# Performance work log

Hardware: AMD Instinct MI355X
Metric: run time of the kernel (lower is better)

## Reference

```python
import jax, jax.numpy as jnp
import numpy as np

N, E, D = 100000, 600000, 128

def setup_inputs() -> dict:
    key = jax.random.key(0)
    ks = jax.random.split(key, 6)
    s = 1.0 / np.sqrt(D)
    return {
        "h": jax.random.normal(ks[0], (N, D), dtype=jnp.float32),
        "edge_index": jax.random.randint(ks[1], (2, E), 0, N, dtype=jnp.int64),
        "Wg": jax.random.normal(ks[2], (2 * D, D), dtype=jnp.float32) * s,
        "bg": jnp.zeros((D,), dtype=jnp.float32),
        "Ws": jax.random.normal(ks[3], (D, D), dtype=jnp.float32) * s,
        "bs": jnp.zeros((D,), dtype=jnp.float32),
        "Wr": jax.random.normal(ks[4], (D, D), dtype=jnp.float32) * s,
        "br": jnp.zeros((D,), dtype=jnp.float32),
    }

def reference(h, edge_index, Wg, bg, Ws, bs, Wr, br):
    send, rec = edge_index[0], edge_index[1]
    h_rec = h[rec]            # [E, D]
    h_send = h[send]          # [E, D]
    # gate: sigmoid(Linear(cat([h_rec, h_send])))  -- split W to avoid concat copy
    gate_in = h_rec @ Wg[:h.shape[1]] + h_send @ Wg[h.shape[1]:] + bg
    eta = jax.nn.sigmoid(gate_in)                      # [E, D]
    h_messages = eta * (h_send @ Ws + bs)              # [E, D]
    h_agg = jax.ops.segment_sum(h_messages, rec, num_segments=h.shape[0])
    return (h @ Wr + br) + h_agg
```

## Files before the change

### kernel.cpp

```cpp
#include <hip/hip_runtime.h>
#include <stdint.h>

#define FD 128

typedef __bf16 bf16x8 __attribute__((ext_vector_type(8)));
typedef unsigned short u16x8 __attribute__((ext_vector_type(8)));
typedef float  f32x16 __attribute__((ext_vector_type(16)));

__device__ __forceinline__ unsigned short f2bf(float f) {
    unsigned u = __float_as_uint(f);
    unsigned r = u + 0x7fffu + ((u >> 16) & 1u);
    return (unsigned short)(r >> 16);
}
__device__ __forceinline__ float bflo(unsigned u) { return __uint_as_float(u << 16); }
__device__ __forceinline__ float bfhi(unsigned u) { return __uint_as_float(u & 0xffff0000u); }

__global__ __launch_bounds__(256) void prep_kernel(
    const float* __restrict__ Wg,
    const float* __restrict__ Ws,
    const float* __restrict__ Wr,
    unsigned short* __restrict__ Wf)
{
    int wid = blockIdx.x * 256 + threadIdx.x;
    if (wid >= 512 * 128) return;
    int j  = wid & 7;
    int l  = (wid >> 3) & 63;
    int kt = (wid >> 9) & 7;
    int ct = wid >> 12;
    int k  = kt * 16 + (l >> 5) * 8 + j;
    int c  = ct * 32 + (l & 31);
    float v;
    if (c < 128)      v = Wg[k * FD + c];
    else if (c < 256) v = Wg[(128 + k) * FD + (c - 128)];
    else if (c < 384) v = Ws[k * FD + (c - 256)];
    else              v = Wr[k * FD + (c - 384)];
    Wf[wid] = f2bf(v);
}

__global__ __launch_bounds__(256, 2) void gemm_kernel(
    const float* __restrict__ h,
    const unsigned short* __restrict__ Wf,
    const float* __restrict__ bg,
    const float* __restrict__ bs,
    const float* __restrict__ br,
    unsigned short* __restrict__ A,
    unsigned short* __restrict__ B,
    unsigned short* __restrict__ S,
    float* __restrict__ out,
    int N)
{
    const int w    = threadIdx.x >> 6;
    const int lane = threadIdx.x & 63;
    const int rb   = blockIdx.x * 32;

    f32x16 acc[4];
    #pragma unroll
    for (int i = 0; i < 4; ++i)
        #pragma unroll
        for (int r = 0; r < 16; ++r) acc[i][r] = 0.0f;

    int arow = rb + (lane & 31);
    if (arow >= N) arow = N - 1;
    const float* aptr = h + (size_t)arow * FD + (lane >> 5) * 8;

    float4 raw[16];
    #pragma unroll
    for (int kt = 0; kt < 8; ++kt) {
        raw[2 * kt]     = *(const float4*)(aptr + kt * 16);
        raw[2 * kt + 1] = *(const float4*)(aptr + kt * 16 + 4);
    }

    bf16x8 afrag[8];
    #pragma unroll
    for (int kt = 0; kt < 8; ++kt) {
        union { u16x8 u; bf16x8 b; } cv;
        float4 f0 = raw[2 * kt];
        float4 f1 = raw[2 * kt + 1];
        cv.u[0] = f2bf(f0.x); cv.u[1] = f2bf(f0.y);
        cv.u[2] = f2bf(f0.z); cv.u[3] = f2bf(f0.w);
        cv.u[4] = f2bf(f1.x); cv.u[5] = f2bf(f1.y);
        cv.u[6] = f2bf(f1.z); cv.u[7] = f2bf(f1.w);
        afrag[kt] = cv.b;
    }

    const unsigned short* bbase = Wf + (size_t)(w * 4 * 8 * 64 + lane) * 8;
    #pragma unroll
    for (int kt = 0; kt < 8; ++kt) {
        #pragma unroll
        for (int i = 0; i < 4; ++i) {
            bf16x8 bfr = *(const bf16x8*)(bbase + (size_t)(i * 8 + kt) * 64 * 8);
            acc[i] = __builtin_amdgcn_mfma_f32_32x32x16_bf16(afrag[kt], bfr, acc[i], 0, 0, 0);
        }
    }

    const int col_l  = lane & 31;
    const int rhalf  = (lane >> 5) * 4;
    #pragma unroll
    for (int i = 0; i < 4; ++i) {
        int col = i * 32 + col_l;
        float bias = (w == 0) ? bg[col] : (w == 2) ? bs[col] : (w == 3) ? br[col] : 0.0f;
        #pragma unroll
        for (int r = 0; r < 16; ++r) {
            int row = rb + (r & 3) + 8 * (r >> 2) + rhalf;
            if (row < N) {
                float v = acc[i][r] + bias;
                size_t off = (size_t)row * FD + col;
                if (w == 0)      A[off] = f2bf(v);
                else if (w == 1) B[off] = f2bf(v);
                else if (w == 2) S[off] = f2bf(v);
                else             out[off] = v;
            }
        }
    }
}

__global__ __launch_bounds__(256) void hist_kernel(
    const int* __restrict__ idx, int* __restrict__ deg, int E)
{
    int e = blockIdx.x * 256 + threadIdx.x;
    if (e >= E) return;
    atomicAdd(&deg[idx[E + e]], 1);
}

__global__ __launch_bounds__(256) void scan1_kernel(
    const int* __restrict__ deg, int* __restrict__ partial, int N)
{
    __shared__ int sh[256];
    int base = blockIdx.x * 1024 + threadIdx.x * 4;
    int s = 0;
    #pragma unroll
    for (int j = 0; j < 4; ++j) s += (base + j < N) ? deg[base + j] : 0;
    sh[threadIdx.x] = s;
    __syncthreads();
    for (int ofs = 128; ofs > 0; ofs >>= 1) {
        if (threadIdx.x < ofs) sh[threadIdx.x] += sh[threadIdx.x + ofs];
        __syncthreads();
    }
    if (threadIdx.x == 0) partial[blockIdx.x] = sh[0];
}

__global__ __launch_bounds__(256) void scan2_kernel(int* __restrict__ partial, int nb)
{
    __shared__ int sh[256];
    int t = threadIdx.x;
    int p = (t < nb) ? partial[t] : 0;
    sh[t] = p;
    __syncthreads();
    for (int ofs = 1; ofs < 256; ofs <<= 1) {
        int x = (t >= ofs) ? sh[t - ofs] : 0;
        __syncthreads();
        sh[t] += x;
        __syncthreads();
    }
    if (t < nb) partial[t] = sh[t] - p;
}

__global__ __launch_bounds__(256) void scan3_kernel(
    int* __restrict__ deg, const int* __restrict__ partial, int N)
{
    __shared__ int sh[256];
    int base = blockIdx.x * 1024 + threadIdx.x * 4;
    int v[4];
    #pragma unroll
    for (int j = 0; j < 4; ++j) v[j] = (base + j < N) ? deg[base + j] : 0;
    int tsum = v[0] + v[1] + v[2] + v[3];
    sh[threadIdx.x] = tsum;
    __syncthreads();
    for (int ofs = 1; ofs < 256; ofs <<= 1) {
        int x = (threadIdx.x >= ofs) ? sh[threadIdx.x - ofs] : 0;
        __syncthreads();
        sh[threadIdx.x] += x;
        __syncthreads();
    }
    int run = partial[blockIdx.x] + sh[threadIdx.x] - tsum;
    #pragma unroll
    for (int j = 0; j < 4; ++j) {
        if (base + j < N) deg[base + j] = run;
        run += v[j];
    }
}

__global__ __launch_bounds__(256) void scatter_kernel(
    const int* __restrict__ idx, int* __restrict__ off,
    int* __restrict__ csr, int E)
{
    int e = blockIdx.x * 256 + threadIdx.x;
    if (e >= E) return;
    int s = idx[e];
    int r = idx[E + e];
    int pos = atomicAdd(&off[r], 1);
    csr[pos] = s;
}

__global__ __launch_bounds__(256) void aggregate_kernel(
    const int* __restrict__ off,
    const int* __restrict__ csr,
    const unsigned* __restrict__ A,
    const unsigned* __restrict__ B,
    const unsigned* __restrict__ S,
    float* __restrict__ out,
    int N)
{
    int r = blockIdx.x * 4 + (threadIdx.x >> 6);
    if (r >= N) return;
    int lane = threadIdx.x & 63;

    int start = (r == 0) ? 0 : off[r - 1];
    int end   = off[r];
    if (start >= end) return;

    unsigned ua = A[(size_t)r * 64 + lane];
    float a0 = bflo(ua), a1 = bfhi(ua);
    float acc0 = 0.0f, acc1 = 0.0f;

    int i = start;
    for (; i + 1 < end; i += 2) {
        int s0 = csr[i], s1 = csr[i + 1];
        unsigned ub0 = B[(size_t)s0 * 64 + lane];
        unsigned us0 = S[(size_t)s0 * 64 + lane];
        unsigned ub1 = B[(size_t)s1 * 64 + lane];
        unsigned us1 = S[(size_t)s1 * 64 + lane];
        float g00 = a0 + bflo(ub0), g01 = a1 + bfhi(ub0);
        float g10 = a0 + bflo(ub1), g11 = a1 + bfhi(ub1);
        acc0 += bflo(us0) * __builtin_amdgcn_rcpf(1.0f + __expf(-g00));
        acc1 += bfhi(us0) * __builtin_amdgcn_rcpf(1.0f + __expf(-g01));
        acc0 += bflo(us1) * __builtin_amdgcn_rcpf(1.0f + __expf(-g10));
        acc1 += bfhi(us1) * __builtin_amdgcn_rcpf(1.0f + __expf(-g11));
    }
    if (i < end) {
        int s0 = csr[i];
        unsigned ub0 = B[(size_t)s0 * 64 + lane];
        unsigned us0 = S[(size_t)s0 * 64 + lane];
        float g00 = a0 + bflo(ub0), g01 = a1 + bfhi(ub0);
        acc0 += bflo(us0) * __builtin_amdgcn_rcpf(1.0f + __expf(-g00));
        acc1 += bfhi(us0) * __builtin_amdgcn_rcpf(1.0f + __expf(-g01));
    }

    float2* o = (float2*)(out + (size_t)r * FD + 2 * lane);
    float2 cur = *o;
    cur.x += acc0;
    cur.y += acc1;
    *o = cur;
}

extern "C" void kernel_launch(void* const* d_in, const int* in_sizes, int n_in,
                              void* d_out, int out_size, void* d_ws, size_t ws_size,
                              hipStream_t stream)
{
    const float* h  = (const float*)d_in[0];
    const int*   ei = (const int*)d_in[1];
    const float* Wg = (const float*)d_in[2];
    const float* bg = (const float*)d_in[3];
    const float* Ws = (const float*)d_in[4];
    const float* bs = (const float*)d_in[5];
    const float* Wr = (const float*)d_in[6];
    const float* br = (const float*)d_in[7];
    float* out = (float*)d_out;

    const int N = in_sizes[0] / FD;
    const int E = in_sizes[1] / 2;

    unsigned short* Wf  = (unsigned short*)d_ws;
    unsigned short* Abf = Wf + 512 * FD;
    unsigned short* Bbf = Abf + (size_t)N * FD;
    unsigned short* Sbf = Bbf + (size_t)N * FD;
    int* deg     = (int*)(Sbf + (size_t)N * FD);
    int* partial = deg + N;
    int* csr     = partial + 256;

    size_t need = (size_t)(512 * FD + 3ull * N * FD) * 2 + ((size_t)N + 256 + E) * 4;
    if (ws_size < need) return;

    const int nb = (N + 1023) / 1024;
    if (nb > 256) return;

    hipMemsetAsync(deg, 0, (size_t)N * 4, stream);

    prep_kernel<<<(512 * FD + 255) / 256, 256, 0, stream>>>(Wg, Ws, Wr, Wf);
    gemm_kernel<<<(N + 31) / 32, 256, 0, stream>>>(h, Wf, bg, bs, br,
                                                   Abf, Bbf, Sbf, out, N);
    hist_kernel<<<(E + 255) / 256, 256, 0, stream>>>(ei, deg, E);
    scan1_kernel<<<nb, 256, 0, stream>>>(deg, partial, N);
    scan2_kernel<<<1, 256, 0, stream>>>(partial, nb);
    scan3_kernel<<<nb, 256, 0, stream>>>(deg, partial, N);
    scatter_kernel<<<(E + 255) / 256, 256, 0, stream>>>(ei, deg, csr, E);
    aggregate_kernel<<<(N + 3) / 4, 256, 0, stream>>>(deg, csr,
                                                      (const unsigned*)Abf,
                                                      (const unsigned*)Bbf,
                                                      (const unsigned*)Sbf,
                                                      out, N);
}
```

Before: 334.0 us.

## Make GEMM kernel persistent with register-resident weight fragments

The node GEMM kernel becomes a grid-stride persistent kernel with 512 blocks. Each wave loads its 32 bf16 weight fragments into registers once and reuses them across many 32-row tiles, where before every block reloaded the weights. A fast path drops the per-row bounds check for full tiles. The change raises register pressure from holding 32 bf16x8 fragments, which may hurt occupancy, and it gives up the latency hiding that came from launching many blocks.

```diff
diff --git a/kernel.cpp b/kernel.cpp
--- a/kernel.cpp
+++ b/kernel.cpp
@@ -51,64 +51,85 @@
 {
     const int w    = threadIdx.x >> 6;
     const int lane = threadIdx.x & 63;
-    const int rb   = blockIdx.x * 32;
-
-    f32x16 acc[4];
-    #pragma unroll
-    for (int i = 0; i < 4; ++i)
-        #pragma unroll
-        for (int r = 0; r < 16; ++r) acc[i][r] = 0.0f;
-
-    int arow = rb + (lane & 31);
-    if (arow >= N) arow = N - 1;
-    const float* aptr = h + (size_t)arow * FD + (lane >> 5) * 8;
-
-    float4 raw[16];
-    #pragma unroll
-    for (int kt = 0; kt < 8; ++kt) {
-        raw[2 * kt]     = *(const float4*)(aptr + kt * 16);
-        raw[2 * kt + 1] = *(const float4*)(aptr + kt * 16 + 4);
-    }
-
-    bf16x8 afrag[8];
-    #pragma unroll
-    for (int kt = 0; kt < 8; ++kt) {
-        union { u16x8 u; bf16x8 b; } cv;
-        float4 f0 = raw[2 * kt];
-        float4 f1 = raw[2 * kt + 1];
-        cv.u[0] = f2bf(f0.x); cv.u[1] = f2bf(f0.y);
-        cv.u[2] = f2bf(f0.z); cv.u[3] = f2bf(f0.w);
-        cv.u[4] = f2bf(f1.x); cv.u[5] = f2bf(f1.y);
-        cv.u[6] = f2bf(f1.z); cv.u[7] = f2bf(f1.w);
-        afrag[kt] = cv.b;
-    }
-
-    const unsigned short* bbase = Wf + (size_t)(w * 4 * 8 * 64 + lane) * 8;
-    #pragma unroll
-    for (int kt = 0; kt < 8; ++kt) {
-        #pragma unroll
-        for (int i = 0; i < 4; ++i) {
-            bf16x8 bfr = *(const bf16x8*)(bbase + (size_t)(i * 8 + kt) * 64 * 8);
-            acc[i] = __builtin_amdgcn_mfma_f32_32x32x16_bf16(afrag[kt], bfr, acc[i], 0, 0, 0);
-        }
-    }
+
+    bf16x8 barr[32];
+    #pragma unroll
+    for (int f = 0; f < 32; ++f)
+        barr[f] = *(const bf16x8*)(Wf + (size_t)((w * 32 + f) * 64 + lane) * 8);
 
     const int col_l  = lane & 31;
     const int rhalf  = (lane >> 5) * 4;
+    float bias[4];
     #pragma unroll
     for (int i = 0; i < 4; ++i) {
         int col = i * 32 + col_l;
-        float bias = (w == 0) ? bg[col] : (w == 2) ? bs[col] : (w == 3) ? br[col] : 0.0f;
+        bias[i] = (w == 0) ? bg[col] : (w == 2) ? bs[col] : (w == 3) ? br[col] : 0.0f;
+    }
+
+    const int stride = gridDim.x * 32;
+    for (int rb = blockIdx.x * 32; rb < N; rb += stride) {
+        int arow = rb + (lane & 31);
+        if (arow >= N) arow = N - 1;
+        const float* aptr = h + (size_t)arow * FD + (lane >> 5) * 8;
+
+        bf16x8 afrag[8];
         #pragma unroll
-        for (int r = 0; r < 16; ++r) {
-            int row = rb + (r & 3) + 8 * (r >> 2) + rhalf;
-            if (row < N) {
-                float v = acc[i][r] + bias;
-                size_t off = (size_t)row * FD + col;
-                if (w == 0)      A[off] = f2bf(v);
-                else if (w == 1) B[off] = f2bf(v);
-                else if (w == 2) S[off] = f2bf(v);
-                else             out[off] = v;
+        for (int kt = 0; kt < 8; ++kt) {
+            float4 f0 = *(const float4*)(aptr + kt * 16);
+            float4 f1 = *(const float4*)(aptr + kt * 16 + 4);
+            union { u16x8 u; bf16x8 b; } cv;
+            cv.u[0] = f2bf(f0.x); cv.u[1] = f2bf(f0.y);
+            cv.u[2] = f2bf(f0.z); cv.u[3] = f2bf(f0.w);
+            cv.u[4] = f2bf(f1.x); cv.u[5] = f2bf(f1.y);
+            cv.u[6] = f2bf(f1.z); cv.u[7] = f2bf(f1.w);
+            afrag[kt] = cv.b;
+        }
+
+        f32x16 acc[4];
+        #pragma unroll
+        for (int i = 0; i < 4; ++i)
+            #pragma unroll
+            for (int r = 0; r < 16; ++r) acc[i][r] = 0.0f;
+
+        #pragma unroll
+        for (int kt = 0; kt < 8; ++kt) {
+            #pragma unroll
+            for (int i = 0; i < 4; ++i)
+                acc[i] = __builtin_amdgcn_mfma_f32_32x32x16_bf16(
+                             afrag[kt], barr[i * 8 + kt], acc[i], 0, 0, 0);
+        }
+
+        if (rb + 32 <= N) {
+            #pragma unroll
+            for (int i = 0; i < 4; ++i) {
+                int col = i * 32 + col_l;
+                #pragma unroll
+                for (int r = 0; r < 16; ++r) {
+                    int row = rb + (r & 3) + 8 * (r >> 2) + rhalf;
+                    float v = acc[i][r] + bias[i];
+                    size_t off = (size_t)row * FD + col;
+                    if (w == 0)      A[off] = f2bf(v);
+                    else if (w == 1) B[off] = f2bf(v);
+                    else if (w == 2) S[off] = f2bf(v);
+                    else             out[off] = v;
+                }
+            }
+        } else {
+            #pragma unroll
+            for (int i = 0; i < 4; ++i) {
+                int col = i * 32 + col_l;
+                #pragma unroll
+                for (int r = 0; r < 16; ++r) {
+                    int row = rb + (r & 3) + 8 * (r >> 2) + rhalf;
+                    if (row < N) {
+                        float v = acc[i][r] + bias[i];
+                        size_t off = (size_t)row * FD + col;
+                        if (w == 0)      A[off] = f2bf(v);
+                        else if (w == 1) B[off] = f2bf(v);
+                        else if (w == 2) S[off] = f2bf(v);
+                        else             out[off] = v;
+                    }
+                }
             }
         }
     }
@@ -277,8 +298,8 @@
     hipMemsetAsync(deg, 0, (size_t)N * 4, stream);
 
     prep_kernel<<<(512 * FD + 255) / 256, 256, 0, stream>>>(Wg, Ws, Wr, Wf);
-    gemm_kernel<<<(N + 31) / 32, 256, 0, stream>>>(h, Wf, bg, bs, br,
-                                                   Abf, Bbf, Sbf, out, N);
+    gemm_kernel<<<512, 256, 0, stream>>>(h, Wf, bg, bs, br,
+                                         Abf, Bbf, Sbf, out, N);
     hist_kernel<<<(E + 255) / 256, 256, 0, stream>>>(ei, deg, E);
     scan1_kernel<<<nb, 256, 0, stream>>>(deg, partial, N);
     scan2_kernel<<<1, 256, 0, stream>>>(partial, nb);
```

Result: no change. 332.2 us (-0.5%).
